# Kernel tuning notes

Measured on AMD Instinct MI355X. Metric: run time of the kernel, lower is better.

The kernel has to match this reference:

```python
import jax, jax.numpy as jnp
import numpy as np

K = 1.0          # manifold curvature parameter (CustomLorentz k)
HEADS = 12
EPS = 1e-6


def add_time(space):
    """Lift space coords onto the hyperboloid: x0 = sqrt(k + ||x_s||^2)."""
    time = jnp.sqrt(K + jnp.sum(space * space, axis=-1, keepdims=True))
    return jnp.concatenate([time, space], axis=-1)


def lorentz_fc_heads(x, W):
    """LorentzFullyConnected with nheads: linear map, split space into heads,
    re-add per-head time coordinate. x: (b,n,F) -> (b,h,n,hd+1)."""
    y = x @ W                                   # (b, n, F)
    b, n, _ = y.shape
    space = y[..., 1:].reshape(b, n, HEADS, -1).transpose(0, 2, 1, 3)  # (b,h,n,hd)
    return add_time(space)


def pairwise_csqdist(q, k):
    """Lorentzian squared distance d^2(x,y) = -2k - 2<x,y>_L, pairwise."""
    inner_space = jnp.einsum('bhid,bhjd->bhij', q[..., 1:], k[..., 1:])
    inner_time = q[..., 0][..., :, None] * k[..., 0][..., None, :]
    inner = inner_space - inner_time            # Lorentz inner product
    return jnp.maximum(-2.0 * K - 2.0 * inner, EPS)


def centroid(v, w):
    """Lorentz centroid: m = w @ v; c = sqrt(k) * m / sqrt(|<m,m>_L|)."""
    m = jnp.einsum('bhij,bhjd->bhid', w, v)     # (b,h,n,hd+1)
    li = jnp.sum(m[..., 1:] ** 2, axis=-1, keepdims=True) - m[..., :1] ** 2
    denom = jnp.sqrt(jnp.maximum(jnp.abs(li), EPS))
    return jnp.sqrt(K) * m / denom


def setup_inputs() -> dict:
    key = jax.random.key(0)
    ks = jax.random.split(key, 5)
    b, n, f = 8, 1024, 769
    x_space = jax.random.normal(ks[0], (b, n, f - 1), dtype=jnp.float32) * 0.5
    x = add_time(x_space)                       # valid hyperboloid points
    init = 0.02
    Wq = jax.random.normal(ks[1], (f, f), dtype=jnp.float32) * init
    Wk = jax.random.normal(ks[2], (f, f), dtype=jnp.float32) * init
    Wv = jax.random.normal(ks[3], (f, f), dtype=jnp.float32) * init
    Wo = jax.random.normal(ks[4], (f, f), dtype=jnp.float32) * init
    return {"x": x, "Wq": Wq, "Wk": Wk, "Wv": Wv, "Wo": Wo}


def reference(x, Wq, Wk, Wv, Wo):
    b, n, _ = x.shape
    q = lorentz_fc_heads(x, Wq)                 # (b,h,n,hd+1)
    k = lorentz_fc_heads(x, Wk)
    v = lorentz_fc_heads(x, Wv)

    d2 = pairwise_csqdist(q, k)                 # (b,h,n,n)
    # score: softmax over query axis (-2) of 1/(1+log(1+d2)), then transpose
    score = jax.nn.softmax(1.0 / (1.0 + jnp.log1p(d2)), axis=-2)
    score = jnp.swapaxes(score, -1, -2)         # rows now sum to 1 over last dim

    attn = centroid(v, score)                   # (b,h,n,hd+1)

    attn_space = attn[..., 1:].transpose(0, 2, 1, 3).reshape(b, n, -1)  # (b,n,h*hd)
    attn_time = attn[..., 0].transpose(0, 2, 1)                         # (b,n,h)
    time_r = jnp.sqrt(jnp.maximum(
        jnp.sum(attn_time ** 2, axis=-1, keepdims=True) - (HEADS - 1) * K, EPS))
    merged = jnp.concatenate([time_r, attn_space], axis=-1)             # (b,n,F)

    # output LorentzFullyConnected (single-head, normalize=False, no dropout at eval)
    y = merged @ Wo
    return add_time(y[..., 1:])
```

## Files before the change

### kernel.cpp

```cpp
#include <hip/hip_runtime.h>
#include <hip/hip_bf16.h>
#include <math.h>

#define HEADS 12
#define NSEQ 1024
#define BATCH 8
#define FDIM 769
#define KP 800
#define NROWS (BATCH*NSEQ)
#define BH (BATCH*HEADS)
#define BHROWS (BH*NSEQ)

typedef __attribute__((ext_vector_type(8))) short bf16x8_t;
typedef __attribute__((ext_vector_type(4))) short bf16x4_t;
typedef __attribute__((ext_vector_type(4))) float f32x4_t;

__device__ __forceinline__ unsigned short f2bf(float f){
    unsigned u = __float_as_uint(f);
    return (unsigned short)((u + 0x7FFFu + ((u >> 16) & 1u)) >> 16);
}

__device__ __forceinline__ float fast_rcp(float x){
    return __builtin_amdgcn_rcpf(x);
}
__device__ __forceinline__ float fast_exp2(float x){
    return __builtin_amdgcn_exp2f(x);
}

__global__ __launch_bounds__(256) void conv_x(const float* __restrict__ x, ushort* __restrict__ xb){
    int idx = blockIdx.x*256 + threadIdx.x;
    int r = idx / 200, c4 = (idx % 200) * 4;
    const float* row = x + (size_t)r * FDIM;
    ushort4 o;
    o.x = (c4+0 < FDIM) ? f2bf(row[c4+0]) : (ushort)0;
    o.y = (c4+1 < FDIM) ? f2bf(row[c4+1]) : (ushort)0;
    o.z = (c4+2 < FDIM) ? f2bf(row[c4+2]) : (ushort)0;
    o.w = (c4+3 < FDIM) ? f2bf(row[c4+3]) : (ushort)0;
    *(ushort4*)(xb + (size_t)r*KP + c4) = o;
}

__global__ __launch_bounds__(256) void conv_w(const float* __restrict__ Wq, const float* __restrict__ Wk,
                                              const float* __restrict__ Wv, const float* __restrict__ Wo,
                                              ushort* __restrict__ WcatT, ushort* __restrict__ WoT){
    int kt = blockIdx.x, nt = blockIdx.y, mat = blockIdx.z;
    const float* W = (mat==0)?Wq:(mat==1)?Wk:(mat==2)?Wv:Wo;
    __shared__ float T[32][33];
    int t = threadIdx.x;
    #pragma unroll
    for (int p=0; p<4; p++){
        int idx = t + p*256;
        int kk = idx>>5, nn = idx&31;
        int kp = kt*32 + kk;
        int srck;
        if (mat < 3) srck = (kp < FDIM) ? kp : -1;
        else         srck = (kp < 768) ? kp+1 : ((kp==768) ? 0 : -1);
        T[kk][nn] = (srck >= 0) ? W[(size_t)srck*FDIM + (nt*32+nn) + 1] : 0.0f;
    }
    __syncthreads();
    ushort* outp = (mat < 3) ? (WcatT + (size_t)mat*768*KP) : WoT;
    #pragma unroll
    for (int p=0; p<4; p++){
        int idx = t + p*256;
        int nl = idx>>5, kk = idx&31;
        outp[(size_t)(nt*32+nl)*KP + kt*32 + kk] = f2bf(T[kk][nl]);
    }
}

__global__ __launch_bounds__(256) void gemm_qkv(const ushort* __restrict__ A, const ushort* __restrict__ Bt,
                                                ushort* __restrict__ qkv, float* __restrict__ tbuf){
    __shared__ __align__(16) ushort As[2][128*32];
    __shared__ __align__(16) ushort Bs[2][128*32];
    const int m0 = blockIdx.x*128, n0 = blockIdx.y*128;
    const int tid = threadIdx.x, lane = tid&63, wave = tid>>6;
    const int wm = wave>>1, wn = wave&1;
    const int g = lane>>4, c = lane&15;

    f32x4_t acc[4][4];
    #pragma unroll
    for (int i=0;i<4;i++)
        #pragma unroll
        for (int j=0;j<4;j++) acc[i][j] = (f32x4_t){0.f,0.f,0.f,0.f};

    bf16x8_t ra[2], rb[2];
    auto LOADS = [&](int kt){
        int k0 = kt*32;
        #pragma unroll
        for (int p=0;p<2;p++){
            int idx = tid + p*256;
            int row = idx>>2, ch = idx&3;
            ra[p] = *(const bf16x8_t*)(A  + (size_t)(m0+row)*KP + k0 + ch*8);
            rb[p] = *(const bf16x8_t*)(Bt + (size_t)(n0+row)*KP + k0 + ch*8);
        }
    };
    auto WRITES = [&](int buf){
        #pragma unroll
        for (int p=0;p<2;p++){
            int idx = tid + p*256;
            int row = idx>>2, ch = idx&3;
            int sw = (ch ^ (row&3))*8;
            *(bf16x8_t*)&As[buf][row*32 + sw] = ra[p];
            *(bf16x8_t*)&Bs[buf][row*32 + sw] = rb[p];
        }
    };

    LOADS(0); WRITES(0); __syncthreads();
    for (int kt=0; kt<25; kt++){
        int cur = kt&1;
        if (kt+1 < 25) LOADS(kt+1);
        bf16x8_t af[4], bf[4];
        #pragma unroll
        for (int mf=0; mf<4; mf++){
            int row = wm*64 + mf*16 + c;
            af[mf] = *(const bf16x8_t*)&As[cur][row*32 + ((g ^ (row&3))*8)];
        }
        #pragma unroll
        for (int nf=0; nf<4; nf++){
            int row = wn*64 + nf*16 + c;
            bf[nf] = *(const bf16x8_t*)&Bs[cur][row*32 + ((g ^ (row&3))*8)];
        }
        #pragma unroll
        for (int mf=0; mf<4; mf++)
            #pragma unroll
            for (int nf=0; nf<4; nf++)
                acc[mf][nf] = __builtin_amdgcn_mfma_f32_16x16x32_bf16(af[mf], bf[nf], acc[mf][nf], 0,0,0);
        if (kt+1 < 25) WRITES(cur^1);
        __syncthreads();
    }

    const int nb = n0 + wn*64;
    const int matv = nb / 768;
    const int hh = (nb % 768) / 64;
    #pragma unroll
    for (int mf=0; mf<4; mf++){
        #pragma unroll
        for (int j=0; j<4; j++){
            int m = m0 + wm*64 + mf*16 + g*4 + j;
            int bb = m >> 10, ns = m & (NSEQ-1);
            size_t rowidx = ((size_t)bb*HEADS + hh)*NSEQ + ns;
            size_t sbase = (size_t)matv*((size_t)BHROWS*64) + rowidx*64;
            float sum = 0.f;
            #pragma unroll
            for (int nf=0; nf<4; nf++){
                float v = acc[mf][nf][j];
                qkv[sbase + nf*16 + c] = f2bf(v);
                sum += v*v;
            }
            sum += __shfl_xor(sum,1,64); sum += __shfl_xor(sum,2,64);
            sum += __shfl_xor(sum,4,64); sum += __shfl_xor(sum,8,64);
            if (c == 0) tbuf[(size_t)matv*BHROWS + rowidx] = sqrtf(1.0f + sum);
        }
    }
}

__global__ __launch_bounds__(256) void transpose_v(const ushort* __restrict__ vsp, ushort* __restrict__ vT){
    const int bh = blockIdx.x >> 3, it128 = blockIdx.x & 7;
    __shared__ ushort T2[64*136];
    const int tid = threadIdx.x;
    {
        int ii = tid>>1, half = tid&1;
        const ushort* src = vsp + ((size_t)bh*NSEQ + it128*128 + ii)*64 + half*32;
        bf16x8_t rr[4];
        #pragma unroll
        for (int p=0;p<4;p++) rr[p] = *(const bf16x8_t*)(src + p*8);
        #pragma unroll
        for (int p=0;p<4;p++)
            #pragma unroll
            for (int e=0;e<8;e++)
                T2[(half*32 + p*8 + e)*136 + ii] = (ushort)rr[p][e];
    }
    __syncthreads();
    {
        int dd = tid>>2, qq = tid&3;
        ushort* dst = vT + ((size_t)bh*64 + dd)*NSEQ + it128*128 + qq*32;
        #pragma unroll
        for (int p=0;p<4;p++)
            *(bf16x8_t*)(dst + p*8) = *(const bf16x8_t*)&T2[dd*136 + qq*32 + p*8];
    }
}

__global__ __launch_bounds__(256, 3) void lorentz_attn(
    const ushort* __restrict__ qsp, const ushort* __restrict__ ksp, const ushort* __restrict__ vT,
    const float* __restrict__ qtg, const float* __restrict__ ktg, const float* __restrict__ vtg,
    ushort* __restrict__ merged, float* __restrict__ ct)
{
    const int lin = blockIdx.x;
    const int bh = lin % BH;
    const int jt = lin / BH;
    const int b = bh / HEADS, h = bh % HEADS;
    const size_t rb = (size_t)bh * NSEQ;

    __shared__ __align__(16) ushort QVbuf[2][9216];
    __shared__ __align__(16) float qts[2][64];
    __shared__ __align__(16) float kts[128];

    const int tid = threadIdx.x, lane = tid&63, wave = tid>>6;
    const int g = lane>>4, c = lane&15;

    ushort* Kst = &QVbuf[0][0];

    bf16x8_t rq[2], rv[2]; float rqt = 0.f, rvt = 0.f;
    const int sr = tid>>2, sch = tid&3;
    auto LOADQV = [&](int it){
        int i0 = it*64;
        const ushort* qp = qsp + (rb + i0 + sr)*64 + sch*16;
        rq[0] = *(const bf16x8_t*)(qp);
        rq[1] = *(const bf16x8_t*)(qp + 8);
        const ushort* vp = vT + ((size_t)bh*64 + sr)*NSEQ + i0 + sch*16;
        rv[0] = *(const bf16x8_t*)(vp);
        rv[1] = *(const bf16x8_t*)(vp + 8);
        if (tid < 64) rqt = qtg[rb + i0 + tid];
        else if (tid < 128) rvt = vtg[rb + i0 + (tid-64)];
    };
    auto WRITEQV = [&](int buf){
        ushort* Qb = &QVbuf[buf][0];
        ushort* Vb = &QVbuf[buf][4096];
        *(bf16x8_t*)&Qb[sr*64 + (((2*sch  ) ^ (sr&7))*8)] = rq[0];
        *(bf16x8_t*)&Qb[sr*64 + (((2*sch+1) ^ (sr&7))*8)] = rq[1];
        int pbase = (sch>>1)*32 + (sch&1)*4;
        int sx = (sr&7)*8;
        #pragma unroll
        for (int s=0; s<4; s++){
            bf16x4_t sl = (s&1) ? (bf16x4_t)__builtin_shufflevector(rv[s>>1], rv[s>>1], 4,5,6,7)
                                : (bf16x4_t)__builtin_shufflevector(rv[s>>1], rv[s>>1], 0,1,2,3);
            *(bf16x4_t*)&Vb[sr*64 + ((pbase + 8*s) ^ sx)] = sl;
        }
        if (tid < 64) qts[buf][tid] = rqt;
        else if (tid < 128){
            int i = tid - 64;
            int p = 32*(i>>5) + 8*((i>>2)&3) + 4*((i>>4)&1) + (i&3);
            Vb[64*64 + p] = f2bf(rvt);
        }
    };

    LOADQV(0);
    {
        int row = tid>>1, half = tid&1;
        const ushort* kp = ksp + (rb + jt*128 + row)*64 + half*32;
        #pragma unroll
        for (int p=0; p<4; p++){
            bf16x8_t kr = *(const bf16x8_t*)(kp + p*8);
            int c8 = half*4 + p;
            *(bf16x8_t*)&Kst[row*64 + ((c8 ^ (row&7))*8)] = kr;
        }
    }
    if (tid < 128) kts[tid] = ktg[rb + jt*128 + tid];
    for (int idx = tid; idx < 2*15*64; idx += 256){
        int bz = idx/(15*64), r2 = idx%(15*64);
        QVbuf[bz][4096 + (65 + (r2>>6))*64 + (r2&63)] = 0;
    }
    __syncthreads();

    bf16x8_t kfrag[2][2]; float kt2e[2];
    #pragma unroll
    for (int jf=0; jf<2; jf++){
        int krow = wave*32 + jf*16 + c;
        kfrag[jf][0] = *(const bf16x8_t*)&Kst[krow*64 + (((  g) ^ (krow&7))*8)];
        kfrag[jf][1] = *(const bf16x8_t*)&Kst[krow*64 + (((4+g) ^ (krow&7))*8)];
        kt2e[jf] = 5.43656365691809f * kts[krow];
    }
    __syncthreads();
    WRITEQV(0);
    __syncthreads();

    f32x4_t acc[2][5];
    #pragma unroll
    for (int jf=0; jf<2; jf++)
        #pragma unroll
        for (int dt=0; dt<5; dt++) acc[jf][dt] = (f32x4_t){0.f,0.f,0.f,0.f};

    for (int it=0; it<16; it++){
        int cur = it&1;
        if (it+1 < 16) LOADQV(it+1);
        ushort* Qc = &QVbuf[cur][0];
        ushort* Vc = &QVbuf[cur][4096];
        #pragma unroll
        for (int ib2=0; ib2<2; ib2++){
            bf16x8_t qf[2][2];
            #pragma unroll
            for (int t=0; t<2; t++){
                int qrow = ib2*32 + t*16 + c;
                qf[t][0] = *(const bf16x8_t*)&Qc[qrow*64 + (((  g) ^ (qrow&7))*8)];
                qf[t][1] = *(const bf16x8_t*)&Qc[qrow*64 + (((4+g) ^ (qrow&7))*8)];
            }
            f32x4_t qt0 = *(const f32x4_t*)&qts[cur][ib2*32 + g*4];
            f32x4_t qt1 = *(const f32x4_t*)&qts[cur][ib2*32 + 16 + g*4];
            bf16x8_t vf[5];
            #pragma unroll
            for (int dt=0; dt<5; dt++){
                int d = dt*16 + c;
                vf[dt] = *(const bf16x8_t*)&Vc[d*64 + ((ib2*32 + g*8) ^ ((d&7)*8))];
            }
            #pragma unroll
            for (int jf=0; jf<2; jf++){
                f32x4_t d0 = (f32x4_t){0.f,0.f,0.f,0.f};
                f32x4_t d1 = (f32x4_t){0.f,0.f,0.f,0.f};
                __builtin_amdgcn_s_setprio(1);
                d0 = __builtin_amdgcn_mfma_f32_16x16x32_bf16(qf[0][0], kfrag[jf][0], d0, 0,0,0);
                d0 = __builtin_amdgcn_mfma_f32_16x16x32_bf16(qf[0][1], kfrag[jf][1], d0, 0,0,0);
                d1 = __builtin_amdgcn_mfma_f32_16x16x32_bf16(qf[1][0], kfrag[jf][0], d1, 0,0,0);
                d1 = __builtin_amdgcn_mfma_f32_16x16x32_bf16(qf[1][1], kfrag[jf][1], d1, 0,0,0);
                __builtin_amdgcn_s_setprio(0);
                float w0[4], w1[4];
                #pragma unroll
                for (int r=0; r<4; r++){
                    float c0 = fmaf(qt0[r], kt2e[jf], -2.718281828f);
                    float s0 = fmaf(d0[r], -5.43656365691809f, c0);
                    float L0 = fmaf((float)__float_as_int(s0), 0x1p-23f, -126.9570f);
                    w0[r] = fast_exp2(fast_rcp(L0) * 2.08136898f);
                    float c1 = fmaf(qt1[r], kt2e[jf], -2.718281828f);
                    float s1 = fmaf(d1[r], -5.43656365691809f, c1);
                    float L1 = fmaf((float)__float_as_int(s1), 0x1p-23f, -126.9570f);
                    w1[r] = fast_exp2(fast_rcp(L1) * 2.08136898f);
                }
                union { __hip_bfloat162 h2[4]; bf16x8_t v8; } uu;
                uu.h2[0] = __float22bfloat162_rn(float2{w0[0], w0[1]});
                uu.h2[1] = __float22bfloat162_rn(float2{w0[2], w0[3]});
                uu.h2[2] = __float22bfloat162_rn(float2{w1[0], w1[1]});
                uu.h2[3] = __float22bfloat162_rn(float2{w1[2], w1[3]});
                bf16x8_t pa = uu.v8;
                __builtin_amdgcn_s_setprio(1);
                #pragma unroll
                for (int dt=0; dt<5; dt++)
                    acc[jf][dt] = __builtin_amdgcn_mfma_f32_16x16x32_bf16(pa, vf[dt], acc[jf][dt], 0,0,0);
                __builtin_amdgcn_s_setprio(0);
            }
        }
        if (it+1 < 16) WRITEQV(cur^1);
        __syncthreads();
    }

    ushort* Ms = &QVbuf[0][0];
    #pragma unroll
    for (int jf=0; jf<2; jf++){
        #pragma unroll
        for (int r=0; r<4; r++){
            float part = 0.f;
            #pragma unroll
            for (int dt=0; dt<4; dt++) part += acc[jf][dt][r]*acc[jf][dt][r];
            part += __shfl_xor(part,1,64); part += __shfl_xor(part,2,64);
            part += __shfl_xor(part,4,64); part += __shfl_xor(part,8,64);
            float tv = acc[jf][4][r];
            float tb = __shfl(tv, lane & 48, 64);
            float li = part - tb*tb;
            float f = rsqrtf(fmaxf(fabsf(li), 1e-6f));
            int jl = wave*32 + jf*16 + g*4 + r;
            #pragma unroll
            for (int dt=0; dt<4; dt++)
                Ms[jl*64 + dt*16 + c] = f2bf(acc[jf][dt][r]*f);
            if (c == 0)
                ct[((size_t)b*NSEQ + jt*128 + jl)*HEADS + h] = tb*f;
        }
    }
    __syncthreads();
    {
        int row = tid>>1, half = tid&1;
        size_t gb = ((size_t)b*NSEQ + jt*128 + row)*KP + h*64 + half*32;
        #pragma unroll
        for (int q4=0; q4<4; q4++)
            *(bf16x8_t*)(merged + gb + q4*8) = *(const bf16x8_t*)&Ms[row*64 + half*32 + q4*8];
    }
}

__global__ __launch_bounds__(256) void gemm_out_k(const ushort* __restrict__ A, const ushort* __restrict__ Bt,
                                                  float* __restrict__ out, float* __restrict__ rowsum){
    __shared__ __align__(16) ushort As[2][128*32];
    __shared__ __align__(16) ushort Bs[2][128*32];
    const int m0 = blockIdx.x*128, n0 = blockIdx.y*128;
    const int tid = threadIdx.x, lane = tid&63, wave = tid>>6;
    const int wm = wave>>1, wn = wave&1;
    const int g = lane>>4, c = lane&15;

    f32x4_t acc[4][4];
    #pragma unroll
    for (int i=0;i<4;i++)
        #pragma unroll
        for (int j=0;j<4;j++) acc[i][j] = (f32x4_t){0.f,0.f,0.f,0.f};

    bf16x8_t ra[2], rb[2];
    auto LOADS = [&](int kt){
        int k0 = kt*32;
        #pragma unroll
        for (int p=0;p<2;p++){
            int idx = tid + p*256;
            int row = idx>>2, ch = idx&3;
            ra[p] = *(const bf16x8_t*)(A  + (size_t)(m0+row)*KP + k0 + ch*8);
            rb[p] = *(const bf16x8_t*)(Bt + (size_t)(n0+row)*KP + k0 + ch*8);
        }
    };
    auto WRITES = [&](int buf){
        #pragma unroll
        for (int p=0;p<2;p++){
            int idx = tid + p*256;
            int row = idx>>2, ch = idx&3;
            int sw = (ch ^ (row&3))*8;
            *(bf16x8_t*)&As[buf][row*32 + sw] = ra[p];
            *(bf16x8_t*)&Bs[buf][row*32 + sw] = rb[p];
        }
    };

    LOADS(0); WRITES(0); __syncthreads();
    for (int kt=0; kt<25; kt++){
        int cur = kt&1;
        if (kt+1 < 25) LOADS(kt+1);
        bf16x8_t af[4], bf[4];
        #pragma unroll
        for (int mf=0; mf<4; mf++){
            int row = wm*64 + mf*16 + c;
            af[mf] = *(const bf16x8_t*)&As[cur][row*32 + ((g ^ (row&3))*8)];
        }
        #pragma unroll
        for (int nf=0; nf<4; nf++){
            int row = wn*64 + nf*16 + c;
            bf[nf] = *(const bf16x8_t*)&Bs[cur][row*32 + ((g ^ (row&3))*8)];
        }
        #pragma unroll
        for (int mf=0; mf<4; mf++)
            #pragma unroll
            for (int nf=0; nf<4; nf++)
                acc[mf][nf] = __builtin_amdgcn_mfma_f32_16x16x32_bf16(af[mf], bf[nf], acc[mf][nf], 0,0,0);
        if (kt+1 < 25) WRITES(cur^1);
        __syncthreads();
    }

    const int slot = blockIdx.y*2 + wn;
    #pragma unroll
    for (int mf=0; mf<4; mf++){
        #pragma unroll
        for (int j=0; j<4; j++){
            int m = m0 + wm*64 + mf*16 + g*4 + j;
            float s = 0.f;
            #pragma unroll
            for (int nf=0; nf<4; nf++){
                float v = acc[mf][nf][j];
                out[(size_t)m*FDIM + 1 + n0 + wn*64 + nf*16 + c] = v;
                s = fmaf(v, v, s);
            }
            s += __shfl_xor(s,1,64); s += __shfl_xor(s,2,64);
            s += __shfl_xor(s,4,64); s += __shfl_xor(s,8,64);
            if (c == 0) rowsum[(size_t)slot*NROWS + m] = s;
        }
    }
}

__global__ __launch_bounds__(256) void time_r_k(const float* __restrict__ ct, ushort* __restrict__ merged){
    int r = blockIdx.x*256 + threadIdx.x;
    float s = 0.f;
    #pragma unroll
    for (int hh=0; hh<HEADS; hh++){
        float t = ct[(size_t)r*HEADS + hh];
        s = fmaf(t, t, s);
    }
    bf16x8_t z = (bf16x8_t){0,0,0,0,0,0,0,0};
    bf16x8_t z0 = z;
    z0[0] = (short)f2bf(sqrtf(fmaxf(s - (float)(HEADS-1), 1e-6f)));
    ushort* dst = merged + (size_t)r*KP + 768;
    *(bf16x8_t*)(dst)      = z0;
    *(bf16x8_t*)(dst + 8)  = z;
    *(bf16x8_t*)(dst + 16) = z;
    *(bf16x8_t*)(dst + 24) = z;
}

__global__ __launch_bounds__(256) void out_time(const float* __restrict__ rowsum, float* __restrict__ out)
{
    int r = blockIdx.x*256 + threadIdx.x;
    float s = 1.0f;
    #pragma unroll
    for (int k=0; k<12; k++) s += rowsum[(size_t)k*NROWS + r];
    out[(size_t)r*FDIM] = sqrtf(s);
}

extern "C" void kernel_launch(void* const* d_in, const int* in_sizes, int n_in,
                              void* d_out, int out_size, void* d_ws, size_t ws_size,
                              hipStream_t stream)
{
    const float* x  = (const float*)d_in[0];
    const float* Wq = (const float*)d_in[1];
    const float* Wk = (const float*)d_in[2];
    const float* Wv = (const float*)d_in[3];
    const float* Wo = (const float*)d_in[4];
    float* out = (float*)d_out;

    char* p = (char*)d_ws;
    ushort* xb     = (ushort*)p; p += (size_t)NROWS*KP*2;
    ushort* WcatT  = (ushort*)p; p += (size_t)2304*KP*2;
    ushort* WoT    = (ushort*)p; p += (size_t)768*KP*2;
    ushort* qkv    = (ushort*)p; p += (size_t)3*BHROWS*64*2;
    float*  tbuf   = (float*)p;  p += (size_t)3*BHROWS*4;
    float*  ct     = (float*)p;  p += (size_t)NROWS*HEADS*4;
    ushort* merged = (ushort*)p; p += (size_t)NROWS*KP*2;
    ushort* vT     = (ushort*)p; p += (size_t)BH*64*NSEQ*2;
    float*  rowsum = (float*)p;  p += (size_t)12*NROWS*4;

    const size_t SP = (size_t)BHROWS*64;

    conv_x<<<6400, 256, 0, stream>>>(x, xb);
    conv_w<<<dim3(25,24,4), 256, 0, stream>>>(Wq, Wk, Wv, Wo, WcatT, WoT);
    gemm_qkv<<<dim3(64,18), 256, 0, stream>>>(xb, WcatT, qkv, tbuf);
    transpose_v<<<768, 256, 0, stream>>>(qkv + 2*SP, vT);
    lorentz_attn<<<768, 256, 0, stream>>>(qkv, qkv + SP, vT,
                                          tbuf, tbuf + BHROWS, tbuf + 2*BHROWS,
                                          merged, ct);
    time_r_k<<<NROWS/256, 256, 0, stream>>>(ct, merged);
    gemm_out_k<<<dim3(64,6), 256, 0, stream>>>(merged, WoT, out, rowsum);
    out_time<<<NROWS/256, 256, 0, stream>>>(rowsum, out);
}
```

Baseline: 160.1 us.

## Fuse V transpose into QKV GEMM epilogue and fold constants in weight math

The QKV GEMM epilogue now writes the V projection directly in transposed (d-major) layout through shared memory. This removes the separate transpose_v kernel and the round-trip of V through global memory, and shrinks the qkv buffer to Q and K only. Separately, the attention weight computation folds the log-scaling multiplier into the fmaf constants, dropping one multiply per score. Costs are extra syncthreads and shared-memory transposes in the V blocks of the GEMM, plus a small change in floating-point rounding.

```diff
diff --git a/kernel.cpp b/kernel.cpp
--- a/kernel.cpp
+++ b/kernel.cpp
@@ -67,9 +67,9 @@
 }
 
 __global__ __launch_bounds__(256) void gemm_qkv(const ushort* __restrict__ A, const ushort* __restrict__ Bt,
-                                                ushort* __restrict__ qkv, float* __restrict__ tbuf){
-    __shared__ __align__(16) ushort As[2][128*32];
-    __shared__ __align__(16) ushort Bs[2][128*32];
+                                                ushort* __restrict__ qkv, ushort* __restrict__ vT,
+                                                float* __restrict__ tbuf){
+    __shared__ __align__(16) ushort SM[2][2][128*32];
     const int m0 = blockIdx.x*128, n0 = blockIdx.y*128;
     const int tid = threadIdx.x, lane = tid&63, wave = tid>>6;
     const int wm = wave>>1, wn = wave&1;
@@ -93,13 +93,15 @@
         }
     };
     auto WRITES = [&](int buf){
+        ushort* As = &SM[buf][0][0];
+        ushort* Bs = &SM[buf][1][0];
         #pragma unroll
         for (int p=0;p<2;p++){
             int idx = tid + p*256;
             int row = idx>>2, ch = idx&3;
             int sw = (ch ^ (row&3))*8;
-            *(bf16x8_t*)&As[buf][row*32 + sw] = ra[p];
-            *(bf16x8_t*)&Bs[buf][row*32 + sw] = rb[p];
+            *(bf16x8_t*)&As[row*32 + sw] = ra[p];
+            *(bf16x8_t*)&Bs[row*32 + sw] = rb[p];
         }
     };
 
@@ -107,16 +109,18 @@
     for (int kt=0; kt<25; kt++){
         int cur = kt&1;
         if (kt+1 < 25) LOADS(kt+1);
+        const ushort* As = &SM[cur][0][0];
+        const ushort* Bs = &SM[cur][1][0];
         bf16x8_t af[4], bf[4];
         #pragma unroll
         for (int mf=0; mf<4; mf++){
             int row = wm*64 + mf*16 + c;
-            af[mf] = *(const bf16x8_t*)&As[cur][row*32 + ((g ^ (row&3))*8)];
+            af[mf] = *(const bf16x8_t*)&As[row*32 + ((g ^ (row&3))*8)];
         }
         #pragma unroll
         for (int nf=0; nf<4; nf++){
             int row = wn*64 + nf*16 + c;
-            bf[nf] = *(const bf16x8_t*)&Bs[cur][row*32 + ((g ^ (row&3))*8)];
+            bf[nf] = *(const bf16x8_t*)&Bs[row*32 + ((g ^ (row&3))*8)];
         }
         #pragma unroll
         for (int mf=0; mf<4; mf++)
@@ -130,51 +134,73 @@
     const int nb = n0 + wn*64;
     const int matv = nb / 768;
     const int hh = (nb % 768) / 64;
-    #pragma unroll
-    for (int mf=0; mf<4; mf++){
-        #pragma unroll
-        for (int j=0; j<4; j++){
-            int m = m0 + wm*64 + mf*16 + g*4 + j;
-            int bb = m >> 10, ns = m & (NSEQ-1);
-            size_t rowidx = ((size_t)bb*HEADS + hh)*NSEQ + ns;
-            size_t sbase = (size_t)matv*((size_t)BHROWS*64) + rowidx*64;
-            float sum = 0.f;
-            #pragma unroll
-            for (int nf=0; nf<4; nf++){
-                float v = acc[mf][nf][j];
-                qkv[sbase + nf*16 + c] = f2bf(v);
-                sum += v*v;
-            }
-            sum += __shfl_xor(sum,1,64); sum += __shfl_xor(sum,2,64);
-            sum += __shfl_xor(sum,4,64); sum += __shfl_xor(sum,8,64);
-            if (c == 0) tbuf[(size_t)matv*BHROWS + rowidx] = sqrtf(1.0f + sum);
-        }
-    }
-}
-
-__global__ __launch_bounds__(256) void transpose_v(const ushort* __restrict__ vsp, ushort* __restrict__ vT){
-    const int bh = blockIdx.x >> 3, it128 = blockIdx.x & 7;
-    __shared__ ushort T2[64*136];
-    const int tid = threadIdx.x;
-    {
-        int ii = tid>>1, half = tid&1;
-        const ushort* src = vsp + ((size_t)bh*NSEQ + it128*128 + ii)*64 + half*32;
-        bf16x8_t rr[4];
-        #pragma unroll
-        for (int p=0;p<4;p++) rr[p] = *(const bf16x8_t*)(src + p*8);
-        #pragma unroll
-        for (int p=0;p<4;p++)
-            #pragma unroll
-            for (int e=0;e<8;e++)
-                T2[(half*32 + p*8 + e)*136 + ii] = (ushort)rr[p][e];
-    }
-    __syncthreads();
-    {
-        int dd = tid>>2, qq = tid&3;
-        ushort* dst = vT + ((size_t)bh*64 + dd)*NSEQ + it128*128 + qq*32;
-        #pragma unroll
-        for (int p=0;p<4;p++)
-            *(bf16x8_t*)(dst + p*8) = *(const bf16x8_t*)&T2[dd*136 + qq*32 + p*8];
+
+    if (matv < 2){
+        #pragma unroll
+        for (int mf=0; mf<4; mf++){
+            #pragma unroll
+            for (int j=0; j<4; j++){
+                int m = m0 + wm*64 + mf*16 + g*4 + j;
+                int bb = m >> 10, ns = m & (NSEQ-1);
+                size_t rowidx = ((size_t)bb*HEADS + hh)*NSEQ + ns;
+                size_t sbase = (size_t)matv*((size_t)BHROWS*64) + rowidx*64;
+                float sum = 0.f;
+                #pragma unroll
+                for (int nf=0; nf<4; nf++){
+                    float v = acc[mf][nf][j];
+                    qkv[sbase + nf*16 + c] = f2bf(v);
+                    sum += v*v;
+                }
+                sum += __shfl_xor(sum,1,64); sum += __shfl_xor(sum,2,64);
+                sum += __shfl_xor(sum,4,64); sum += __shfl_xor(sum,8,64);
+                if (c == 0) tbuf[(size_t)matv*BHROWS + rowidx] = sqrtf(1.0f + sum);
+            }
+        }
+    } else {
+        #pragma unroll
+        for (int mf=0; mf<4; mf++){
+            #pragma unroll
+            for (int j=0; j<4; j++){
+                int m = m0 + wm*64 + mf*16 + g*4 + j;
+                int bb = m >> 10, ns = m & (NSEQ-1);
+                size_t rowidx = ((size_t)bb*HEADS + hh)*NSEQ + ns;
+                float sum = 0.f;
+                #pragma unroll
+                for (int nf=0; nf<4; nf++){
+                    float v = acc[mf][nf][j];
+                    sum = fmaf(v, v, sum);
+                }
+                sum += __shfl_xor(sum,1,64); sum += __shfl_xor(sum,2,64);
+                sum += __shfl_xor(sum,4,64); sum += __shfl_xor(sum,8,64);
+                if (c == 0) tbuf[2*(size_t)BHROWS + rowidx] = sqrtf(1.0f + sum);
+            }
+        }
+        ushort* T = &SM[0][0][0];
+        const int bb = m0 >> 10, ns0 = m0 & (NSEQ-1);
+        const int hh0 = (n0 % 768) / 64;
+        #pragma unroll
+        for (int w2=0; w2<2; w2++){
+            __syncthreads();
+            if (wn == w2){
+                #pragma unroll
+                for (int mf=0; mf<4; mf++)
+                    #pragma unroll
+                    for (int j=0; j<4; j++){
+                        int lm = wm*64 + mf*16 + g*4 + j;
+                        #pragma unroll
+                        for (int nf=0; nf<4; nf++)
+                            T[(nf*16+c)*136 + lm] = f2bf(acc[mf][nf][j]);
+                    }
+            }
+            __syncthreads();
+            {
+                int dd = tid>>2, qq = tid&3;
+                size_t gbase = ((size_t)(bb*HEADS + hh0 + w2)*64 + dd)*NSEQ + ns0 + qq*32;
+                #pragma unroll
+                for (int p2=0; p2<4; p2++)
+                    *(bf16x8_t*)(vT + gbase + p2*8) = *(const bf16x8_t*)&T[dd*136 + qq*32 + p2*8];
+            }
+        }
     }
 }
 
@@ -305,12 +331,12 @@
                 for (int r=0; r<4; r++){
                     float c0 = fmaf(qt0[r], kt2e[jf], -2.718281828f);
                     float s0 = fmaf(d0[r], -5.43656365691809f, c0);
-                    float L0 = fmaf((float)__float_as_int(s0), 0x1p-23f, -126.9570f);
-                    w0[r] = fast_exp2(fast_rcp(L0) * 2.08136898f);
+                    float L0 = fmaf((float)__float_as_int(s0), 5.727461e-8f, -60.996868f);
+                    w0[r] = fast_exp2(fast_rcp(L0));
                     float c1 = fmaf(qt1[r], kt2e[jf], -2.718281828f);
                     float s1 = fmaf(d1[r], -5.43656365691809f, c1);
-                    float L1 = fmaf((float)__float_as_int(s1), 0x1p-23f, -126.9570f);
-                    w1[r] = fast_exp2(fast_rcp(L1) * 2.08136898f);
+                    float L1 = fmaf((float)__float_as_int(s1), 5.727461e-8f, -60.996868f);
+                    w1[r] = fast_exp2(fast_rcp(L1));
                 }
                 union { __hip_bfloat162 h2[4]; bf16x8_t v8; } uu;
                 uu.h2[0] = __float22bfloat162_rn(float2{w0[0], w0[1]});
@@ -484,7 +510,7 @@
     ushort* xb     = (ushort*)p; p += (size_t)NROWS*KP*2;
     ushort* WcatT  = (ushort*)p; p += (size_t)2304*KP*2;
     ushort* WoT    = (ushort*)p; p += (size_t)768*KP*2;
-    ushort* qkv    = (ushort*)p; p += (size_t)3*BHROWS*64*2;
+    ushort* qkv    = (ushort*)p; p += (size_t)2*BHROWS*64*2;
     float*  tbuf   = (float*)p;  p += (size_t)3*BHROWS*4;
     float*  ct     = (float*)p;  p += (size_t)NROWS*HEADS*4;
     ushort* merged = (ushort*)p; p += (size_t)NROWS*KP*2;
@@ -495,8 +521,7 @@
 
     conv_x<<<6400, 256, 0, stream>>>(x, xb);
     conv_w<<<dim3(25,24,4), 256, 0, stream>>>(Wq, Wk, Wv, Wo, WcatT, WoT);
-    gemm_qkv<<<dim3(64,18), 256, 0, stream>>>(xb, WcatT, qkv, tbuf);
-    transpose_v<<<768, 256, 0, stream>>>(qkv + 2*SP, vT);
+    gemm_qkv<<<dim3(64,18), 256, 0, stream>>>(xb, WcatT, qkv, vT, tbuf);
     lorentz_attn<<<768, 256, 0, stream>>>(qkv, qkv + SP, vT,
                                           tbuf, tbuf + BHROWS, tbuf + 2*BHROWS,
                                           merged, ct);
```

New measurement: 172.6 us. +7.8%, slower.
